# Kernel tuning notes

Measured on AMD Instinct MI355X. Metric: run time of the kernel, lower is better.

The kernel has to match this reference:

```python
import jax, jax.numpy as jnp
import numpy as np

H = 512
IN = 64
OUT = 1


def _lstm_layer(x, W_ih, W_hh, b_ih, b_hh):
    # x: (B, T, D). PyTorch gate order: i, f, g, o stacked along 4H.
    B, T, _ = x.shape
    Hd = W_hh.shape[1]
    # Precompute input contribution for all timesteps (one big GEMM).
    xg = jnp.einsum('btd,gd->btg', x, W_ih) + b_ih + b_hh  # (B, T, 4H)

    def step(carry, xg_t):
        h, c = carry
        gates = xg_t + h @ W_hh.T  # (B, 4H)
        i, f, g, o = jnp.split(gates, 4, axis=-1)
        i = jax.nn.sigmoid(i)
        f = jax.nn.sigmoid(f)
        g = jnp.tanh(g)
        o = jax.nn.sigmoid(o)
        c = f * c + i * g
        h = o * jnp.tanh(c)
        return (h, c), h

    h0 = jnp.zeros((B, Hd), x.dtype)
    c0 = jnp.zeros((B, Hd), x.dtype)
    (_, _), hs = jax.lax.scan(step, (h0, c0), jnp.swapaxes(xg, 0, 1))
    return jnp.swapaxes(hs, 0, 1)  # (B, T, H)


def setup_inputs() -> dict:
    key = jax.random.key(0)
    ks = jax.random.split(key, 12)
    s = 1.0 / np.sqrt(H)  # PyTorch LSTM init scale
    u = lambda k, shp: jax.random.uniform(k, shp, jnp.float32, -s, s)
    return {
        'x': jax.random.normal(ks[0], (64, 512, IN), jnp.float32),
        'W_ih0': u(ks[1], (4 * H, IN)),
        'W_hh0': u(ks[2], (4 * H, H)),
        'b_ih0': u(ks[3], (4 * H,)),
        'b_hh0': u(ks[4], (4 * H,)),
        'W_ih1': u(ks[5], (4 * H, H)),
        'W_hh1': u(ks[6], (4 * H, H)),
        'b_ih1': u(ks[7], (4 * H,)),
        'b_hh1': u(ks[8], (4 * H,)),
        'fc_w': u(ks[9], (OUT, H)),
        'fc_b': u(ks[10], (OUT,)),
    }


def reference(x, W_ih0, W_hh0, b_ih0, b_hh0, W_ih1, W_hh1, b_ih1, b_hh1, fc_w, fc_b):
    # Two stacked LSTM layers (eval mode: inter-layer dropout disabled),
    # then linear head on the last timestep's hidden state.
    h1 = _lstm_layer(x, W_ih0, W_hh0, b_ih0, b_hh0)   # (B, T, H)
    h2 = _lstm_layer(h1, W_ih1, W_hh1, b_ih1, b_hh1)  # (B, T, H)
    return h2[:, -1, :] @ fc_w.T + fc_b               # (B, OUT)
```

## Files before the change

kernel.cpp:

```cpp
#include <hip/hip_runtime.h>
#include <stdint.h>

static constexpr int NBLK = 256;
static constexpr int NTHR = 256;
static constexpr int Hd   = 512;
static constexpr int Td   = 512;
static constexpr int IND  = 64;
static constexpr int Bd   = 64;
static constexpr int HBUF = Bd * Hd;
static constexpr int HR   = 520;
static constexpr unsigned POIS32 = 0xAAAAAAAAu;

typedef __attribute__((ext_vector_type(8))) short short8;
typedef __attribute__((ext_vector_type(4))) float f4;

#define MFMA(a, b, c) __builtin_amdgcn_mfma_f32_16x16x32_bf16((a), (b), (c), 0, 0, 0)

__device__ __forceinline__ uint64_t ld_agent64(const uint64_t* p) {
  return __hip_atomic_load((uint64_t*)p, __ATOMIC_RELAXED, __HIP_MEMORY_SCOPE_AGENT);
}
__device__ __forceinline__ void st_agent32(unsigned* p, unsigned v) {
  __hip_atomic_store(p, v, __ATOMIC_RELAXED, __HIP_MEMORY_SCOPE_AGENT);
}
__device__ __forceinline__ float sigmoidf_(float v) { return 1.0f / (1.0f + __expf(-v)); }
__device__ __forceinline__ float tanhf_(float v) {
  v = fminf(15.0f, fmaxf(-15.0f, v));
  float e = __expf(2.0f * v);
  return (e - 1.0f) / (e + 1.0f);
}
__device__ __forceinline__ unsigned short bf16_rne(float f) {
  unsigned u = __float_as_uint(f);
  unsigned r = u + 0x7FFFu + ((u >> 16) & 1u);
  return (unsigned short)(r >> 16);
}
__device__ __forceinline__ unsigned pack_h(float h) {
  unsigned short hb = bf16_rne(h);
  float hf = __uint_as_float((unsigned)hb << 16);
  unsigned short lb = bf16_rne(h - hf);
  unsigned pk = ((unsigned)hb << 16) | (unsigned)lb;
  if (pk == POIS32) pk ^= 1u;
  return pk;
}
__device__ __forceinline__ int good64(uint64_t w) {
  return (int)((unsigned)w != POIS32) & (int)((unsigned)(w >> 32) != POIS32);
}
__device__ __forceinline__ void spin_check16(const uint64_t* base, int tid, uint64_t* tmp) {
  int guard = 0;
  for (;;) {
    unsigned ok = 1;
    #pragma unroll
    for (int k = 0; k < 16; ++k) ok &= (unsigned)good64(tmp[k]);
    if (ok || ++guard > (1 << 16)) break;
    __builtin_amdgcn_s_sleep(1);
    #pragma unroll
    for (int k = 0; k < 16; ++k) tmp[k] = ld_agent64(base + k * 256 + tid);
  }
}

__global__ __launch_bounds__(256) void split_x_kernel(
    const float* __restrict__ x, short* __restrict__ xhi, short* __restrict__ xlo) {
  int i = blockIdx.x * 256 + threadIdx.x;
  float4 v = ((const float4*)x)[i];
  float f[4] = {v.x, v.y, v.z, v.w};
  unsigned h[4], l[4];
  #pragma unroll
  for (int e = 0; e < 4; ++e) {
    unsigned short hb = bf16_rne(f[e]);
    float r = f[e] - __uint_as_float((unsigned)hb << 16);
    h[e] = hb; l[e] = bf16_rne(r);
  }
  uint2 hp = {h[0] | (h[1] << 16), h[2] | (h[3] << 16)};
  uint2 lp = {l[0] | (l[1] << 16), l[2] | (l[3] << 16)};
  *(uint2*)&xhi[i * 4] = hp;
  *(uint2*)&xlo[i * 4] = lp;
}

__global__ __launch_bounds__(NTHR, 1) void lstm2_flow(
    const float* __restrict__ Wih0, const float* __restrict__ Whh0,
    const float* __restrict__ bih0, const float* __restrict__ bhh0,
    const float* __restrict__ Wih1, const float* __restrict__ Whh1,
    const float* __restrict__ bih1, const float* __restrict__ bhh1,
    const float* __restrict__ fcw,  const float* __restrict__ fcb,
    float* __restrict__ out,
    const short* __restrict__ xhi, const short* __restrict__ xlo,
    unsigned* __restrict__ h1, unsigned* __restrict__ h2)
{
  __shared__ short hiA1[16 * HR];
  __shared__ short loA1[16 * HR];
  __shared__ short hiA2[16 * HR];
  __shared__ short loA2[16 * HR];
  __shared__ short Blo[4 * 16 * 64 * 8];
  __shared__ float g_lds[4][16][16];
  __shared__ float red[NTHR];

  const int tid  = threadIdx.x;
  const int wave = tid >> 6;
  const int lane = tid & 63;
  const int nB   = lane & 15;
  const int q    = lane >> 4;
  const int mA   = lane & 15;

  const int xcd   = blockIdx.x & 7;
  const int layer = xcd >> 2;
  const int mt    = xcd & 3;
  const int jt    = blockIdx.x >> 3;
  const int jBase = jt * 16;
  const int bBase = mt * 16;
  const int wrow  = wave * Hd + jBase + nB;

  const int pm = tid >> 4;
  const int pn = tid & 15;

  if (layer == 0) {
    short8 bh[18], bl[18];
    {
      const float* Wh = Whh0 + (size_t)wrow * Hd;
      const float* Wi = Wih0 + (size_t)wrow * IND;
      #pragma unroll
      for (int kt = 0; kt < 18; ++kt) {
        const float* src = (kt < 16) ? (Wh + kt * 32 + q * 8) : (Wi + (kt - 16) * 32 + q * 8);
        float wv[8];
        *(float4*)&wv[0] = *(const float4*)src;
        *(float4*)&wv[4] = *(const float4*)(src + 4);
        #pragma unroll
        for (int j = 0; j < 8; ++j) {
          unsigned short hb = bf16_rne(wv[j]);
          float r = wv[j] - __uint_as_float((unsigned)hb << 16);
          ((short*)&bh[kt])[j] = (short)hb;
          ((short*)&bl[kt])[j] = (short)bf16_rne(r);
        }
      }
    }
    float bias[4];
    #pragma unroll
    for (int g4 = 0; g4 < 4; ++g4) {
      int r = g4 * Hd + jBase + pn;
      bias[g4] = bih0[r] + bhh0[r];
    }
    float c1 = 0.0f;

    for (int t = 0; t < Td; ++t) {
      const uint64_t* s1 = (const uint64_t*)(h1 + (size_t)((t >= 1) ? t - 1 : 0) * HBUF)
                           + bBase * 256;
      uint64_t tmp[16];
      if (t >= 1) {
        #pragma unroll
        for (int k = 0; k < 16; ++k) tmp[k] = ld_agent64(s1 + k * 256 + tid);
      }

      f4 a0 = {0.f,0.f,0.f,0.f}, a1 = {0.f,0.f,0.f,0.f}, a2 = {0.f,0.f,0.f,0.f};
      f4 d0 = {0.f,0.f,0.f,0.f}, d1 = {0.f,0.f,0.f,0.f}, d2 = {0.f,0.f,0.f,0.f};
      {
        const size_t xb = ((size_t)(bBase + mA) * Td + t) * IND;
        short8 x0h = *(const short8*)&xhi[xb + q * 8];
        short8 x0l = *(const short8*)&xlo[xb + q * 8];
        short8 x1h = *(const short8*)&xhi[xb + 32 + q * 8];
        short8 x1l = *(const short8*)&xlo[xb + 32 + q * 8];
        a0 = MFMA(x0h, bh[16], a0); a1 = MFMA(x0h, bl[16], a1); a2 = MFMA(x0l, bh[16], a2);
        d0 = MFMA(x1h, bh[17], d0); d1 = MFMA(x1h, bl[17], d1); d2 = MFMA(x1l, bh[17], d2);
      }
      if (t >= 1) {
        spin_check16(s1, tid, tmp);
        #pragma unroll
        for (int k = 0; k < 16; ++k) {
          unsigned p0 = (unsigned)tmp[k], p1 = (unsigned)(tmp[k] >> 32);
          *(unsigned*)&hiA1[k * HR + tid * 2] = __builtin_amdgcn_perm(p1, p0, 0x07060302u);
          *(unsigned*)&loA1[k * HR + tid * 2] = __builtin_amdgcn_perm(p1, p0, 0x05040100u);
        }
      }
      __syncthreads();

      if (t >= 1) {
        #pragma unroll
        for (int kt = 0; kt < 16; kt += 2) {
          short8 ah0 = *(const short8*)&hiA1[mA * HR + kt * 32 + q * 8];
          short8 al0 = *(const short8*)&loA1[mA * HR + kt * 32 + q * 8];
          short8 ah1 = *(const short8*)&hiA1[mA * HR + (kt + 1) * 32 + q * 8];
          short8 al1 = *(const short8*)&loA1[mA * HR + (kt + 1) * 32 + q * 8];
          a0 = MFMA(ah0, bh[kt], a0);
          d0 = MFMA(ah1, bh[kt + 1], d0);
          a1 = MFMA(ah0, bl[kt], a1);
          d1 = MFMA(ah1, bl[kt + 1], d1);
          a2 = MFMA(al0, bh[kt], a2);
          d2 = MFMA(al1, bh[kt + 1], d2);
        }
      }
      #pragma unroll
      for (int r2 = 0; r2 < 4; ++r2)
        g_lds[wave][q * 4 + r2][nB] =
            (a0[r2] + d0[r2]) + (a1[r2] + d1[r2]) + (a2[r2] + d2[r2]);
      __syncthreads();

      {
        float pi = g_lds[0][pm][pn] + bias[0];
        float pf = g_lds[1][pm][pn] + bias[1];
        float pg = g_lds[2][pm][pn] + bias[2];
        float po = g_lds[3][pm][pn] + bias[3];
        float ig = sigmoidf_(pi), fg = sigmoidf_(pf), gg = tanhf_(pg), og = sigmoidf_(po);
        c1 = fmaf(fg, c1, ig * gg);
        float h = og * tanhf_(c1);
        st_agent32(h1 + (size_t)t * HBUF + (bBase + pm) * Hd + jBase + pn, pack_h(h));
      }
    }

    if (blockIdx.x == 0) {
      const int b = tid >> 2, q4 = tid & 3;
      float sum = 0.0f;
      #pragma unroll
      for (int ch = 0; ch < 4; ++ch) {
        const uint64_t* hp = (const uint64_t*)(h2 + (size_t)(Td - 1) * HBUF) + b * 256 + q4 * 64 + ch * 16;
        uint64_t w[16];
        int guard = 0;
        for (;;) {
          unsigned ok = 1;
          #pragma unroll
          for (int u = 0; u < 16; ++u) w[u] = ld_agent64(hp + u);
          #pragma unroll
          for (int u = 0; u < 16; ++u) ok &= (unsigned)good64(w[u]);
          if (ok || ++guard > (1 << 17)) break;
          __builtin_amdgcn_s_sleep(1);
        }
        #pragma unroll
        for (int u = 0; u < 16; ++u) {
          int cw = q4 * 64 + ch * 16 + u;
          unsigned plo = (unsigned)w[u], phi = (unsigned)(w[u] >> 32);
          float vlo = __uint_as_float(plo & 0xFFFF0000u) + __uint_as_float(plo << 16);
          float vhi = __uint_as_float(phi & 0xFFFF0000u) + __uint_as_float(phi << 16);
          sum = fmaf(vlo, fcw[2 * cw], fmaf(vhi, fcw[2 * cw + 1], sum));
        }
      }
      red[tid] = sum;
      __syncthreads();
      if (q4 == 0) out[b] = red[tid] + red[tid + 1] + red[tid + 2] + red[tid + 3] + fcb[0];
    }
  } else {
    short8 bh[32], bl[16];
    {
      const float* Wi = Wih1 + (size_t)wrow * Hd;
      const float* Wh = Whh1 + (size_t)wrow * Hd;
      #pragma unroll
      for (int kt = 0; kt < 16; ++kt) {
        float wv[8];
        *(float4*)&wv[0] = *(const float4*)(Wi + kt * 32 + q * 8);
        *(float4*)&wv[4] = *(const float4*)(Wi + kt * 32 + q * 8 + 4);
        #pragma unroll
        for (int j = 0; j < 8; ++j) {
          unsigned short hb = bf16_rne(wv[j]);
          float r = wv[j] - __uint_as_float((unsigned)hb << 16);
          ((short*)&bh[kt])[j] = (short)hb;
          ((short*)&bl[kt])[j] = (short)bf16_rne(r);
        }
      }
      #pragma unroll
      for (int kt = 0; kt < 16; ++kt) {
        float wv[8];
        *(float4*)&wv[0] = *(const float4*)(Wh + kt * 32 + q * 8);
        *(float4*)&wv[4] = *(const float4*)(Wh + kt * 32 + q * 8 + 4);
        short lo8[8];
        #pragma unroll
        for (int j = 0; j < 8; ++j) {
          unsigned short hb = bf16_rne(wv[j]);
          float r = wv[j] - __uint_as_float((unsigned)hb << 16);
          ((short*)&bh[16 + kt])[j] = (short)hb;
          lo8[j] = (short)bf16_rne(r);
        }
        *(short8*)&Blo[((wave * 16 + kt) * 64 + lane) * 8] = *(short8*)lo8;
      }
    }
    float bias[4];
    #pragma unroll
    for (int g4 = 0; g4 < 4; ++g4) {
      int r = g4 * Hd + jBase + pn;
      bias[g4] = bih1[r] + bhh1[r];
    }
    float c2 = 0.0f;
    __syncthreads();

    for (int t = 0; t < Td; ++t) {
      const uint64_t* s1 = (const uint64_t*)(h1 + (size_t)t * HBUF) + bBase * 256;
      const uint64_t* s2 = (const uint64_t*)(h2 + (size_t)((t >= 1) ? t - 1 : 0) * HBUF)
                           + bBase * 256;

      uint64_t t1[16], t2[16];
      #pragma unroll
      for (int k = 0; k < 16; ++k) t1[k] = ld_agent64(s1 + k * 256 + tid);
      if (t >= 1) {
        #pragma unroll
        for (int k = 0; k < 16; ++k) t2[k] = ld_agent64(s2 + k * 256 + tid);
      }

      spin_check16(s1, tid, t1);
      #pragma unroll
      for (int k = 0; k < 16; ++k) {
        unsigned p0 = (unsigned)t1[k], p1 = (unsigned)(t1[k] >> 32);
        *(unsigned*)&hiA1[k * HR + tid * 2] = __builtin_amdgcn_perm(p1, p0, 0x07060302u);
        *(unsigned*)&loA1[k * HR + tid * 2] = __builtin_amdgcn_perm(p1, p0, 0x05040100u);
      }
      if (t >= 1) {
        spin_check16(s2, tid, t2);
        #pragma unroll
        for (int k = 0; k < 16; ++k) {
          unsigned q0 = (unsigned)t2[k], q1 = (unsigned)(t2[k] >> 32);
          *(unsigned*)&hiA2[k * HR + tid * 2] = __builtin_amdgcn_perm(q1, q0, 0x07060302u);
          *(unsigned*)&loA2[k * HR + tid * 2] = __builtin_amdgcn_perm(q1, q0, 0x05040100u);
        }
      }
      __syncthreads();

      f4 a0 = {0.f,0.f,0.f,0.f}, a1 = {0.f,0.f,0.f,0.f}, a2 = {0.f,0.f,0.f,0.f};
      f4 d0 = {0.f,0.f,0.f,0.f}, d1 = {0.f,0.f,0.f,0.f}, d2 = {0.f,0.f,0.f,0.f};
      #pragma unroll
      for (int kt = 0; kt < 16; kt += 2) {
        short8 ah0 = *(const short8*)&hiA1[mA * HR + kt * 32 + q * 8];
        short8 al0 = *(const short8*)&loA1[mA * HR + kt * 32 + q * 8];
        short8 ah1 = *(const short8*)&hiA1[mA * HR + (kt + 1) * 32 + q * 8];
        short8 al1 = *(const short8*)&loA1[mA * HR + (kt + 1) * 32 + q * 8];
        a0 = MFMA(ah0, bh[kt], a0);
        d0 = MFMA(ah1, bh[kt + 1], d0);
        a1 = MFMA(ah0, bl[kt], a1);
        d1 = MFMA(ah1, bl[kt + 1], d1);
        a2 = MFMA(al0, bh[kt], a2);
        d2 = MFMA(al1, bh[kt + 1], d2);
      }
      if (t >= 1) {
        #pragma unroll
        for (int kt = 0; kt < 16; kt += 2) {
          short8 ah0  = *(const short8*)&hiA2[mA * HR + kt * 32 + q * 8];
          short8 al0  = *(const short8*)&loA2[mA * HR + kt * 32 + q * 8];
          short8 wlo0 = *(const short8*)&Blo[((wave * 16 + kt) * 64 + lane) * 8];
          short8 ah1  = *(const short8*)&hiA2[mA * HR + (kt + 1) * 32 + q * 8];
          short8 al1  = *(const short8*)&loA2[mA * HR + (kt + 1) * 32 + q * 8];
          short8 wlo1 = *(const short8*)&Blo[((wave * 16 + kt + 1) * 64 + lane) * 8];
          a0 = MFMA(ah0, bh[16 + kt], a0);
          d0 = MFMA(ah1, bh[16 + kt + 1], d0);
          a1 = MFMA(ah0, wlo0, a1);
          d1 = MFMA(ah1, wlo1, d1);
          a2 = MFMA(al0, bh[16 + kt], a2);
          d2 = MFMA(al1, bh[16 + kt + 1], d2);
        }
      }
      #pragma unroll
      for (int r2 = 0; r2 < 4; ++r2)
        g_lds[wave][q * 4 + r2][nB] =
            (a0[r2] + d0[r2]) + (a1[r2] + d1[r2]) + (a2[r2] + d2[r2]);
      __syncthreads();

      {
        float pi = g_lds[0][pm][pn] + bias[0];
        float pf = g_lds[1][pm][pn] + bias[1];
        float pg = g_lds[2][pm][pn] + bias[2];
        float po = g_lds[3][pm][pn] + bias[3];
        float ig = sigmoidf_(pi), fg = sigmoidf_(pf), gg = tanhf_(pg), og = sigmoidf_(po);
        c2 = fmaf(fg, c2, ig * gg);
        float h = og * tanhf_(c2);
        st_agent32(h2 + (size_t)t * HBUF + (bBase + pm) * Hd + jBase + pn, pack_h(h));
      }
    }
  }
}

extern "C" void kernel_launch(void* const* d_in, const int* in_sizes, int n_in,
                              void* d_out, int out_size, void* d_ws, size_t ws_size,
                              hipStream_t stream) {
  const float* x    = (const float*)d_in[0];
  const float* Wih0 = (const float*)d_in[1];
  const float* Whh0 = (const float*)d_in[2];
  const float* bih0 = (const float*)d_in[3];
  const float* bhh0 = (const float*)d_in[4];
  const float* Wih1 = (const float*)d_in[5];
  const float* Whh1 = (const float*)d_in[6];
  const float* bih1 = (const float*)d_in[7];
  const float* bhh1 = (const float*)d_in[8];
  const float* fcw  = (const float*)d_in[9];
  const float* fcb  = (const float*)d_in[10];

  char* base = (char*)d_ws;
  short* xhi = (short*)base;
  const size_t xplane = (size_t)Bd * Td * IND;
  short* xlo = xhi + xplane;
  unsigned* h1 = (unsigned*)(xlo + xplane);
  unsigned* h2 = h1 + (size_t)Td * HBUF;

  const size_t need = 4 * xplane + 2 * (size_t)Td * HBUF * 4;
  if (ws_size < need) return;

  hipLaunchKernelGGL(split_x_kernel, dim3((unsigned)(xplane / 4 / 256)), dim3(256), 0, stream,
                     x, xhi, xlo);
  hipLaunchKernelGGL(lstm2_flow, dim3(NBLK), dim3(NTHR), 0, stream,
                     Wih0, Whh0, bih0, bhh0, Wih1, Whh1, bih1, bhh1, fcw, fcb,
                     (float*)d_out, xhi, xlo, h1, h2);
}
```

Baseline: 2.293 ms.

## Split recurrent GEMM across waves by K-slice instead of by gate

Result: faster. 2.159 ms (-5.8%).

```diff
diff --git a/kernel.cpp b/kernel.cpp
--- a/kernel.cpp
+++ b/kernel.cpp
@@ -54,6 +54,18 @@
     __builtin_amdgcn_s_sleep(1);
     #pragma unroll
     for (int k = 0; k < 16; ++k) tmp[k] = ld_agent64(base + k * 256 + tid);
+  }
+}
+__device__ __forceinline__ void load_split8(const float* src, short8* hi, short8* lo) {
+  float wv[8];
+  *(float4*)&wv[0] = *(const float4*)src;
+  *(float4*)&wv[4] = *(const float4*)(src + 4);
+  #pragma unroll
+  for (int j = 0; j < 8; ++j) {
+    unsigned short hb = bf16_rne(wv[j]);
+    float r = wv[j] - __uint_as_float((unsigned)hb << 16);
+    ((short*)hi)[j] = (short)hb;
+    ((short*)lo)[j] = (short)bf16_rne(r);
   }
 }
 
@@ -90,7 +102,7 @@
   __shared__ short hiA2[16 * HR];
   __shared__ short loA2[16 * HR];
   __shared__ short Blo[4 * 16 * 64 * 8];
-  __shared__ float g_lds[4][16][16];
+  __shared__ float gp[4][4][16][17];
   __shared__ float red[NTHR];
 
   const int tid  = threadIdx.x;
@@ -106,29 +118,26 @@
   const int jt    = blockIdx.x >> 3;
   const int jBase = jt * 16;
   const int bBase = mt * 16;
-  const int wrow  = wave * Hd + jBase + nB;
 
   const int pm = tid >> 4;
   const int pn = tid & 15;
 
   if (layer == 0) {
-    short8 bh[18], bl[18];
-    {
-      const float* Wh = Whh0 + (size_t)wrow * Hd;
-      const float* Wi = Wih0 + (size_t)wrow * IND;
-      #pragma unroll
-      for (int kt = 0; kt < 18; ++kt) {
-        const float* src = (kt < 16) ? (Wh + kt * 32 + q * 8) : (Wi + (kt - 16) * 32 + q * 8);
-        float wv[8];
-        *(float4*)&wv[0] = *(const float4*)src;
-        *(float4*)&wv[4] = *(const float4*)(src + 4);
-        #pragma unroll
-        for (int j = 0; j < 8; ++j) {
-          unsigned short hb = bf16_rne(wv[j]);
-          float r = wv[j] - __uint_as_float((unsigned)hb << 16);
-          ((short*)&bh[kt])[j] = (short)hb;
-          ((short*)&bl[kt])[j] = (short)bf16_rne(r);
-        }
+    short8 bhhh[4][4], bhhl[4][4];
+    short8 bxh[4], bxl[4];
+    #pragma unroll
+    for (int g = 0; g < 4; ++g) {
+      #pragma unroll
+      for (int kk = 0; kk < 4; ++kk) {
+        const float* src = Whh0 + (size_t)(g * Hd + jBase + nB) * Hd + (wave * 4 + kk) * 32 + q * 8;
+        load_split8(src, &bhhh[g][kk], &bhhl[g][kk]);
+      }
+    }
+    if (wave < 2) {
+      #pragma unroll
+      for (int g = 0; g < 4; ++g) {
+        const float* src = Wih0 + (size_t)(g * Hd + jBase + nB) * IND + wave * 32 + q * 8;
+        load_split8(src, &bxh[g], &bxl[g]);
       }
     }
     float bias[4];
@@ -148,17 +157,21 @@
         for (int k = 0; k < 16; ++k) tmp[k] = ld_agent64(s1 + k * 256 + tid);
       }
 
-      f4 a0 = {0.f,0.f,0.f,0.f}, a1 = {0.f,0.f,0.f,0.f}, a2 = {0.f,0.f,0.f,0.f};
-      f4 d0 = {0.f,0.f,0.f,0.f}, d1 = {0.f,0.f,0.f,0.f}, d2 = {0.f,0.f,0.f,0.f};
-      {
-        const size_t xb = ((size_t)(bBase + mA) * Td + t) * IND;
-        short8 x0h = *(const short8*)&xhi[xb + q * 8];
-        short8 x0l = *(const short8*)&xlo[xb + q * 8];
-        short8 x1h = *(const short8*)&xhi[xb + 32 + q * 8];
-        short8 x1l = *(const short8*)&xlo[xb + 32 + q * 8];
-        a0 = MFMA(x0h, bh[16], a0); a1 = MFMA(x0h, bl[16], a1); a2 = MFMA(x0l, bh[16], a2);
-        d0 = MFMA(x1h, bh[17], d0); d1 = MFMA(x1h, bl[17], d1); d2 = MFMA(x1l, bh[17], d2);
-      }
+      f4 aH[4] = {{0.f,0.f,0.f,0.f},{0.f,0.f,0.f,0.f},{0.f,0.f,0.f,0.f},{0.f,0.f,0.f,0.f}};
+      f4 aL[4] = {{0.f,0.f,0.f,0.f},{0.f,0.f,0.f,0.f},{0.f,0.f,0.f,0.f},{0.f,0.f,0.f,0.f}};
+
+      if (wave < 2) {
+        const size_t xb = ((size_t)(bBase + mA) * Td + t) * IND + wave * 32 + q * 8;
+        short8 xh = *(const short8*)&xhi[xb];
+        short8 xl = *(const short8*)&xlo[xb];
+        #pragma unroll
+        for (int g = 0; g < 4; ++g) {
+          aH[g] = MFMA(xh, bxh[g], aH[g]);
+          aL[g] = MFMA(xh, bxl[g], aL[g]);
+          aL[g] = MFMA(xl, bxh[g], aL[g]);
+        }
+      }
+
       if (t >= 1) {
         spin_check16(s1, tid, tmp);
         #pragma unroll
@@ -167,40 +180,42 @@
           *(unsigned*)&hiA1[k * HR + tid * 2] = __builtin_amdgcn_perm(p1, p0, 0x07060302u);
           *(unsigned*)&loA1[k * HR + tid * 2] = __builtin_amdgcn_perm(p1, p0, 0x05040100u);
         }
-      }
-      __syncthreads();
-
-      if (t >= 1) {
-        #pragma unroll
-        for (int kt = 0; kt < 16; kt += 2) {
-          short8 ah0 = *(const short8*)&hiA1[mA * HR + kt * 32 + q * 8];
-          short8 al0 = *(const short8*)&loA1[mA * HR + kt * 32 + q * 8];
-          short8 ah1 = *(const short8*)&hiA1[mA * HR + (kt + 1) * 32 + q * 8];
-          short8 al1 = *(const short8*)&loA1[mA * HR + (kt + 1) * 32 + q * 8];
-          a0 = MFMA(ah0, bh[kt], a0);
-          d0 = MFMA(ah1, bh[kt + 1], d0);
-          a1 = MFMA(ah0, bl[kt], a1);
-          d1 = MFMA(ah1, bl[kt + 1], d1);
-          a2 = MFMA(al0, bh[kt], a2);
-          d2 = MFMA(al1, bh[kt + 1], d2);
-        }
-      }
-      #pragma unroll
-      for (int r2 = 0; r2 < 4; ++r2)
-        g_lds[wave][q * 4 + r2][nB] =
-            (a0[r2] + d0[r2]) + (a1[r2] + d1[r2]) + (a2[r2] + d2[r2]);
+        #pragma unroll
+        for (int kk = 0; kk < 4; ++kk) {
+          const int kt = wave * 4 + kk;
+          short8 ah = *(const short8*)&hiA1[mA * HR + kt * 32 + q * 8];
+          short8 al = *(const short8*)&loA1[mA * HR + kt * 32 + q * 8];
+          #pragma unroll
+          for (int g = 0; g < 4; ++g) {
+            aH[g] = MFMA(ah, bhhh[g][kk], aH[g]);
+            aL[g] = MFMA(ah, bhhl[g][kk], aL[g]);
+            aL[g] = MFMA(al, bhhh[g][kk], aL[g]);
+          }
+        }
+      }
+      #pragma unroll
+      for (int g = 0; g < 4; ++g) {
+        #pragma unroll
+        for (int r2 = 0; r2 < 4; ++r2)
+          gp[wave][g][q * 4 + r2][nB] = aH[g][r2] + aL[g][r2];
+      }
       __syncthreads();
 
       {
-        float pi = g_lds[0][pm][pn] + bias[0];
-        float pf = g_lds[1][pm][pn] + bias[1];
-        float pg = g_lds[2][pm][pn] + bias[2];
-        float po = g_lds[3][pm][pn] + bias[3];
+        float pi = bias[0], pf = bias[1], pg = bias[2], po = bias[3];
+        #pragma unroll
+        for (int w = 0; w < 4; ++w) {
+          pi += gp[w][0][pm][pn];
+          pf += gp[w][1][pm][pn];
+          pg += gp[w][2][pm][pn];
+          po += gp[w][3][pm][pn];
+        }
         float ig = sigmoidf_(pi), fg = sigmoidf_(pf), gg = tanhf_(pg), og = sigmoidf_(po);
         c1 = fmaf(fg, c1, ig * gg);
         float h = og * tanhf_(c1);
         st_agent32(h1 + (size_t)t * HBUF + (bBase + pm) * Hd + jBase + pn, pack_h(h));
       }
+      __syncthreads();
     }
 
     if (blockIdx.x == 0) {
@@ -234,37 +249,18 @@
       if (q4 == 0) out[b] = red[tid] + red[tid + 1] + red[tid + 2] + red[tid + 3] + fcb[0];
     }
   } else {
-    short8 bh[32], bl[16];
-    {
-      const float* Wi = Wih1 + (size_t)wrow * Hd;
-      const float* Wh = Whh1 + (size_t)wrow * Hd;
-      #pragma unroll
-      for (int kt = 0; kt < 16; ++kt) {
-        float wv[8];
-        *(float4*)&wv[0] = *(const float4*)(Wi + kt * 32 + q * 8);
-        *(float4*)&wv[4] = *(const float4*)(Wi + kt * 32 + q * 8 + 4);
-        #pragma unroll
-        for (int j = 0; j < 8; ++j) {
-          unsigned short hb = bf16_rne(wv[j]);
-          float r = wv[j] - __uint_as_float((unsigned)hb << 16);
-          ((short*)&bh[kt])[j] = (short)hb;
-          ((short*)&bl[kt])[j] = (short)bf16_rne(r);
-        }
-      }
-      #pragma unroll
-      for (int kt = 0; kt < 16; ++kt) {
-        float wv[8];
-        *(float4*)&wv[0] = *(const float4*)(Wh + kt * 32 + q * 8);
-        *(float4*)&wv[4] = *(const float4*)(Wh + kt * 32 + q * 8 + 4);
-        short lo8[8];
-        #pragma unroll
-        for (int j = 0; j < 8; ++j) {
-          unsigned short hb = bf16_rne(wv[j]);
-          float r = wv[j] - __uint_as_float((unsigned)hb << 16);
-          ((short*)&bh[16 + kt])[j] = (short)hb;
-          lo8[j] = (short)bf16_rne(r);
-        }
-        *(short8*)&Blo[((wave * 16 + kt) * 64 + lane) * 8] = *(short8*)lo8;
+    short8 bihh[4][4], bihl[4][4], bhhh[4][4];
+    #pragma unroll
+    for (int g = 0; g < 4; ++g) {
+      #pragma unroll
+      for (int kk = 0; kk < 4; ++kk) {
+        const int kt = wave * 4 + kk;
+        const float* srcI = Wih1 + (size_t)(g * Hd + jBase + nB) * Hd + kt * 32 + q * 8;
+        load_split8(srcI, &bihh[g][kk], &bihl[g][kk]);
+        const float* srcH = Whh1 + (size_t)(g * Hd + jBase + nB) * Hd + kt * 32 + q * 8;
+        short8 hlo;
+        load_split8(srcH, &bhhh[g][kk], &hlo);
+        *(short8*)&Blo[((g * 16 + kt) * 64 + lane) * 8] = hlo;
       }
     }
     float bias[4];
@@ -280,7 +276,6 @@
       const uint64_t* s1 = (const uint64_t*)(h1 + (size_t)t * HBUF) + bBase * 256;
       const uint64_t* s2 = (const uint64_t*)(h2 + (size_t)((t >= 1) ? t - 1 : 0) * HBUF)
                            + bBase * 256;
-
       uint64_t t1[16], t2[16];
       #pragma unroll
       for (int k = 0; k < 16; ++k) t1[k] = ld_agent64(s1 + k * 256 + tid);
@@ -288,6 +283,9 @@
         #pragma unroll
         for (int k = 0; k < 16; ++k) t2[k] = ld_agent64(s2 + k * 256 + tid);
       }
+
+      f4 aH[4] = {{0.f,0.f,0.f,0.f},{0.f,0.f,0.f,0.f},{0.f,0.f,0.f,0.f},{0.f,0.f,0.f,0.f}};
+      f4 aL[4] = {{0.f,0.f,0.f,0.f},{0.f,0.f,0.f,0.f},{0.f,0.f,0.f,0.f},{0.f,0.f,0.f,0.f}};
 
       spin_check16(s1, tid, t1);
       #pragma unroll
@@ -296,6 +294,18 @@
         *(unsigned*)&hiA1[k * HR + tid * 2] = __builtin_amdgcn_perm(p1, p0, 0x07060302u);
         *(unsigned*)&loA1[k * HR + tid * 2] = __builtin_amdgcn_perm(p1, p0, 0x05040100u);
       }
+      #pragma unroll
+      for (int kk = 0; kk < 4; ++kk) {
+        const int kt = wave * 4 + kk;
+        short8 ah = *(const short8*)&hiA1[mA * HR + kt * 32 + q * 8];
+        short8 al = *(const short8*)&loA1[mA * HR + kt * 32 + q * 8];
+        #pragma unroll
+        for (int g = 0; g < 4; ++g) {
+          aH[g] = MFMA(ah, bihh[g][kk], aH[g]);
+          aL[g] = MFMA(ah, bihl[g][kk], aL[g]);
+          aL[g] = MFMA(al, bihh[g][kk], aL[g]);
+        }
+      }
       if (t >= 1) {
         spin_check16(s2, tid, t2);
         #pragma unroll
@@ -304,57 +314,43 @@
           *(unsigned*)&hiA2[k * HR + tid * 2] = __builtin_amdgcn_perm(q1, q0, 0x07060302u);
           *(unsigned*)&loA2[k * HR + tid * 2] = __builtin_amdgcn_perm(q1, q0, 0x05040100u);
         }
-      }
-      __syncthreads();
-
-      f4 a0 = {0.f,0.f,0.f,0.f}, a1 = {0.f,0.f,0.f,0.f}, a2 = {0.f,0.f,0.f,0.f};
-      f4 d0 = {0.f,0.f,0.f,0.f}, d1 = {0.f,0.f,0.f,0.f}, d2 = {0.f,0.f,0.f,0.f};
-      #pragma unroll
-      for (int kt = 0; kt < 16; kt += 2) {
-        short8 ah0 = *(const short8*)&hiA1[mA * HR + kt * 32 + q * 8];
-        short8 al0 = *(const short8*)&loA1[mA * HR + kt * 32 + q * 8];
-        short8 ah1 = *(const short8*)&hiA1[mA * HR + (kt + 1) * 32 + q * 8];
-        short8 al1 = *(const short8*)&loA1[mA * HR + (kt + 1) * 32 + q * 8];
-        a0 = MFMA(ah0, bh[kt], a0);
-        d0 = MFMA(ah1, bh[kt + 1], d0);
-        a1 = MFMA(ah0, bl[kt], a1);
-        d1 = MFMA(ah1, bl[kt + 1], d1);
-        a2 = MFMA(al0, bh[kt], a2);
-        d2 = MFMA(al1, bh[kt + 1], d2);
-      }
-      if (t >= 1) {
-        #pragma unroll
-        for (int kt = 0; kt < 16; kt += 2) {
-          short8 ah0  = *(const short8*)&hiA2[mA * HR + kt * 32 + q * 8];
-          short8 al0  = *(const short8*)&loA2[mA * HR + kt * 32 + q * 8];
-          short8 wlo0 = *(const short8*)&Blo[((wave * 16 + kt) * 64 + lane) * 8];
-          short8 ah1  = *(const short8*)&hiA2[mA * HR + (kt + 1) * 32 + q * 8];
-          short8 al1  = *(const short8*)&loA2[mA * HR + (kt + 1) * 32 + q * 8];
-          short8 wlo1 = *(const short8*)&Blo[((wave * 16 + kt + 1) * 64 + lane) * 8];
-          a0 = MFMA(ah0, bh[16 + kt], a0);
-          d0 = MFMA(ah1, bh[16 + kt + 1], d0);
-          a1 = MFMA(ah0, wlo0, a1);
-          d1 = MFMA(ah1, wlo1, d1);
-          a2 = MFMA(al0, bh[16 + kt], a2);
-          d2 = MFMA(al1, bh[16 + kt + 1], d2);
-        }
-      }
-      #pragma unroll
-      for (int r2 = 0; r2 < 4; ++r2)
-        g_lds[wave][q * 4 + r2][nB] =
-            (a0[r2] + d0[r2]) + (a1[r2] + d1[r2]) + (a2[r2] + d2[r2]);
+        #pragma unroll
+        for (int kk = 0; kk < 4; ++kk) {
+          const int kt = wave * 4 + kk;
+          short8 ah = *(const short8*)&hiA2[mA * HR + kt * 32 + q * 8];
+          short8 al = *(const short8*)&loA2[mA * HR + kt * 32 + q * 8];
+          #pragma unroll
+          for (int g = 0; g < 4; ++g) {
+            short8 wlo = *(const short8*)&Blo[((g * 16 + kt) * 64 + lane) * 8];
+            aH[g] = MFMA(ah, bhhh[g][kk], aH[g]);
+            aL[g] = MFMA(ah, wlo, aL[g]);
+            aL[g] = MFMA(al, bhhh[g][kk], aL[g]);
+          }
+        }
+      }
+      #pragma unroll
+      for (int g = 0; g < 4; ++g) {
+        #pragma unroll
+        for (int r2 = 0; r2 < 4; ++r2)
+          gp[wave][g][q * 4 + r2][nB] = aH[g][r2] + aL[g][r2];
+      }
       __syncthreads();
 
       {
-        float pi = g_lds[0][pm][pn] + bias[0];
-        float pf = g_lds[1][pm][pn] + bias[1];
-        float pg = g_lds[2][pm][pn] + bias[2];
-        float po = g_lds[3][pm][pn] + bias[3];
+        float pi = bias[0], pf = bias[1], pg = bias[2], po = bias[3];
+        #pragma unroll
+        for (int w = 0; w < 4; ++w) {
+          pi += gp[w][0][pm][pn];
+          pf += gp[w][1][pm][pn];
+          pg += gp[w][2][pm][pn];
+          po += gp[w][3][pm][pn];
+        }
         float ig = sigmoidf_(pi), fg = sigmoidf_(pf), gg = tanhf_(pg), og = sigmoidf_(po);
         c2 = fmaf(fg, c2, ig * gg);
         float h = og * tanhf_(c2);
         st_agent32(h2 + (size_t)t * HBUF + (bBase + pm) * Hd + jBase + pn, pack_h(h));
       }
+      __syncthreads();
     }
   }
 }
```
